# Performance work log

Hardware: AMD Instinct MI355X
Metric: run time of the kernel (lower is better)

Reference implementation:

```python
import jax, jax.numpy as jnp
import numpy as np

HIDDEN = 2048
NUM_HEADS = 16
NUM_KV_HEADS = 4
HEAD_DIM = HIDDEN // NUM_HEADS  # 128
GROUP = NUM_HEADS // NUM_KV_HEADS  # 4
SCALE = HEAD_DIM ** -0.5


def setup_inputs() -> dict:
    key = jax.random.key(0)
    ks = jax.random.split(key, 9)
    B, S = 2, 2048
    kv_dim = HEAD_DIM * NUM_KV_HEADS
    std = HIDDEN ** -0.5
    return {
        "x": jax.random.normal(ks[0], (B, S, HIDDEN), dtype=jnp.float32),
        "Wq": jax.random.normal(ks[1], (HIDDEN, HIDDEN), dtype=jnp.float32) * std,
        "bq": jnp.zeros((HIDDEN,), dtype=jnp.float32),
        "Wk": jax.random.normal(ks[2], (HIDDEN, kv_dim), dtype=jnp.float32) * std,
        "bk": jnp.zeros((kv_dim,), dtype=jnp.float32),
        "Wv": jax.random.normal(ks[3], (HIDDEN, kv_dim), dtype=jnp.float32) * std,
        "bv": jnp.zeros((kv_dim,), dtype=jnp.float32),
        "Wo": jax.random.normal(ks[4], (HIDDEN, HIDDEN), dtype=jnp.float32) * std,
        "bo": jnp.zeros((HIDDEN,), dtype=jnp.float32),
    }


def reference(x, Wq, bq, Wk, bk, Wv, bv, Wo, bo):
    B, S, _ = x.shape
    # projections
    q = (x @ Wq + bq).reshape(B, S, NUM_KV_HEADS, GROUP, HEAD_DIM)  # grouped query heads
    k = (x @ Wk + bk).reshape(B, S, NUM_KV_HEADS, HEAD_DIM)
    v = (x @ Wv + bv).reshape(B, S, NUM_KV_HEADS, HEAD_DIM)
    # scores: [B, Hkv, G, Sq, Sk] -- same math as repeat_interleave of K/V over G,
    # but K/V are broadcast over the group axis instead of materialized.
    attn = jnp.einsum("bqhgd,bkhd->bhgqk", q, k) * SCALE
    attn = jax.nn.softmax(attn, axis=-1)
    out = jnp.einsum("bhgqk,bkhd->bqhgd", attn, v).reshape(B, S, HIDDEN)
    return out @ Wo + bo
```

## Files before the change

### kernel.cpp

```cpp
#include <hip/hip_runtime.h>


#define SEQ    2048
#define HIDDEN 2048

typedef __attribute__((ext_vector_type(8))) short v8s;
typedef __attribute__((ext_vector_type(4))) float v4f;

#define MFMA16(a,b,c) __builtin_amdgcn_mfma_f32_16x16x32_bf16((a),(b),(c),0,0,0)

__device__ __forceinline__ ushort f2b(float f){
  unsigned u = __float_as_uint(f);
  u += 0x7fffu + ((u >> 16) & 1u);
  return (ushort)(u >> 16);
}

__device__ __forceinline__ void gload16(const void* g, void* l){
  __builtin_amdgcn_global_load_lds((const __attribute__((address_space(1))) void*)g,
                                   (__attribute__((address_space(3))) void*)l, 16, 0, 0);
}

#define WAIT_VM0   0x0F70
#define WAIT_LGKM0 0xC07F

__global__ void k_conv(const float* __restrict__ in, ushort* __restrict__ out, int n){
  int i = (blockIdx.x*256 + threadIdx.x)*4;
  if (i >= n) return;
  float4 f = *(const float4*)(in + i);
  ushort4 u; u.x=f2b(f.x); u.y=f2b(f.y); u.z=f2b(f.z); u.w=f2b(f.w);
  *(ushort4*)(out + i) = u;
}

__global__ void k_tconv(const float* __restrict__ in, ushort* __restrict__ out,
                        int rows, int cols){
  __shared__ float t[32][33];
  int tx = threadIdx.x & 31, ty = threadIdx.x >> 5;
  int c0 = blockIdx.x*32, r0 = blockIdx.y*32;
#pragma unroll
  for (int i=0;i<4;i++) t[ty+i*8][tx] = in[(size_t)(r0+ty+i*8)*cols + c0+tx];
  __syncthreads();
#pragma unroll
  for (int i=0;i<4;i++) out[(size_t)(c0+ty+i*8)*rows + r0+tx] = f2b(t[tx][ty+i*8]);
}

__global__ void k_tv(const ushort* __restrict__ vb, ushort* __restrict__ vT){
  __shared__ ushort t[32][33];
  int tx = threadIdx.x & 31, ty = threadIdx.x >> 5;
  int s0 = blockIdx.x*32, d0 = blockIdx.y*32, bh = blockIdx.z;
  int b = bh >> 2, h = bh & 3;
  const ushort* src = vb + (size_t)b*SEQ*512 + h*128;
#pragma unroll
  for (int i=0;i<4;i++) t[ty+i*8][tx] = src[(size_t)(s0+ty+i*8)*512 + d0+tx];
  __syncthreads();
  ushort* dst = vT + (size_t)bh*128*SEQ;
#pragma unroll
  for (int i=0;i<4;i++) dst[(size_t)(d0+ty+i*8)*SEQ + s0+tx] = t[tx][ty+i*8];
}

#define GEMM_MAIN(A_, Bt_, K_)                                                        \
  __shared__ ushort sA[128*32], sB[128*32];                                           \
  const int tid = threadIdx.x, lane = tid & 63, wid = tid >> 6;                       \
  const int wm = wid >> 1, wn = wid & 1, lm = lane & 15, q8 = (lane >> 4)*8;          \
  const int rowB = blockIdx.y*128, colB = blockIdx.x*128;                             \
  v4f acc[4][4] = {};                                                                 \
  for (int k0 = 0; k0 < (K_); k0 += 32){                                              \
    _Pragma("unroll")                                                                 \
    for (int it=0; it<2; it++){                                                       \
      int c = tid + it*256;                                                           \
      gload16((A_)  + (size_t)(rowB + (c>>2))*(K_) + k0 + (c&3)*8, (char*)sA + c*16); \
      gload16((Bt_) + (size_t)(colB + (c>>2))*(K_) + k0 + (c&3)*8, (char*)sB + c*16); \
    }                                                                                 \
    __syncthreads();                                                                  \
    v8s af[4], bfr[4];                                                                \
    _Pragma("unroll")                                                                 \
    for (int i=0;i<4;i++){                                                            \
      af[i]  = *(const v8s*)(sA + (wm*64 + i*16 + lm)*32 + q8);                       \
      bfr[i] = *(const v8s*)(sB + (wn*64 + i*16 + lm)*32 + q8);                       \
    }                                                                                 \
    _Pragma("unroll")                                                                 \
    for (int i=0;i<4;i++)                                                             \
      _Pragma("unroll")                                                               \
      for (int j=0;j<4;j++) acc[i][j] = MFMA16(af[i], bfr[j], acc[i][j]);             \
    __syncthreads();                                                                  \
  }                                                                                   \
  const int quad = lane >> 4;

__global__ __launch_bounds__(256) void k_gemm_qkv(
    const ushort* __restrict__ A, const ushort* __restrict__ Bt,
    const float* __restrict__ bq, const float* __restrict__ bk, const float* __restrict__ bv,
    ushort* __restrict__ qb, ushort* __restrict__ kb, ushort* __restrict__ vb){
  GEMM_MAIN(A, Bt, HIDDEN)
#pragma unroll
  for (int i=0;i<4;i++)
#pragma unroll
  for (int j=0;j<4;j++){
    int col = colB + wn*64 + j*16 + lm;
#pragma unroll
    for (int r=0;r<4;r++){
      int row = rowB + wm*64 + i*16 + quad*4 + r;
      float v = acc[i][j][r];
      if (col < 2048)      qb[(size_t)row*2048 + col]        = f2b(v + bq[col]);
      else if (col < 2560) kb[(size_t)row*512 + (col-2048)]  = f2b(v + bk[col-2048]);
      else                 vb[(size_t)row*512 + (col-2560)]  = f2b(v + bv[col-2560]);
    }
  }
}

__global__ __launch_bounds__(256) void k_gemm_out(
    const ushort* __restrict__ A, const ushort* __restrict__ Bt,
    const float* __restrict__ bo, float* __restrict__ out){
  GEMM_MAIN(A, Bt, HIDDEN)
#pragma unroll
  for (int i=0;i<4;i++)
#pragma unroll
  for (int j=0;j<4;j++){
    int col = colB + wn*64 + j*16 + lm;
#pragma unroll
    for (int r=0;r<4;r++){
      int row = rowB + wm*64 + i*16 + quad*4 + r;
      out[(size_t)row*2048 + col] = acc[i][j][r] + bo[col];
    }
  }
}

__global__ __launch_bounds__(512, 1) void k_attn(
    const ushort* __restrict__ qb, const ushort* __restrict__ kb,
    const ushort* __restrict__ vT, ushort* __restrict__ Ob){
  __shared__ ushort sK[2][64*128];
  __shared__ ushort sV[2][128*64];
  __shared__ ushort sP[8][2048];
  const int tid = threadIdx.x, lane = tid & 63, w = tid >> 6;
  const int lm = lane & 15, quad = lane >> 4, q8 = quad*8;
  const int pair = blockIdx.x & 7;
  const int hkv = pair & 3, b = pair >> 2;
  const int qt = (blockIdx.x >> 3) & 7, g = blockIdx.x >> 6;
  const int head = hkv*4 + g;
  const float C = 0.08838834764831845f * 1.4426950408889634f;

  const ushort* kbb = kb + (size_t)b*SEQ*512 + hkv*128;
  const ushort* vbb = vT + (size_t)(b*4+hkv)*128*SEQ;

  const int kk = lane >> 4, ksw = lane & 15;
  const int dd = lane >> 3, vsw = lane & 7;

#define STAGE_K(t, buf) { _Pragma("unroll") for (int i=0;i<2;i++){                     \
    int c = w*2 + i; int key = c*4 + kk; int wd = ksw ^ (key & 15);                    \
    gload16(kbb + (size_t)((t)*64 + key)*512 + wd*8, &sK[buf][c*512 + lane*8]); } }
#define STAGE_V(t, buf) { _Pragma("unroll") for (int i=0;i<2;i++){                     \
    int c = w*2 + i; int drow = c*8 + dd; int wd = vsw ^ dd;                           \
    gload16(vbb + (size_t)drow*SEQ + (t)*64 + wd*8, &sV[buf][c*512 + lane*8]); } }

  v8s qf[2][4];
#pragma unroll
  for (int rb=0; rb<2; rb++)
#pragma unroll
    for (int ks=0; ks<4; ks++)
      qf[rb][ks] = *(const v8s*)(qb + (size_t)(b*SEQ + qt*256 + w*32 + rb*16 + lm)*HIDDEN
                                    + head*128 + ks*32 + q8);

  v4f o[2][8] = {};
  float lreg[2] = {0.f, 0.f};

  STAGE_K(0, 0)
  STAGE_V(0, 0)
  __builtin_amdgcn_s_waitcnt(WAIT_VM0);
  __syncthreads();

  for (int t=0; t<32; t++){
    const int cur = t & 1;
    if (t < 31) STAGE_K(t+1, cur^1)

    v8s kf[4][4];
#pragma unroll
    for (int kt=0; kt<4; kt++)
#pragma unroll
      for (int ks=0; ks<4; ks++)
        kf[kt][ks] = *(const v8s*)(&sK[cur][(kt*16+lm)*128 + ((ks*4+quad)^lm)*8]);

    v4f sacc[2][4] = {};
    __builtin_amdgcn_s_setprio(1);
#pragma unroll
    for (int ks=0; ks<4; ks++)
#pragma unroll
      for (int kt=0; kt<4; kt++)
#pragma unroll
        for (int rb=0; rb<2; rb++)
          sacc[rb][kt] = MFMA16(kf[kt][ks], qf[rb][ks], sacc[rb][kt]);
    __builtin_amdgcn_s_setprio(0);

#pragma unroll
    for (int rb=0; rb<2; rb++){
      float rs = 0.f;
#pragma unroll
      for (int kt=0; kt<4; kt++){
        float p0 = __builtin_amdgcn_exp2f(sacc[rb][kt][0]*C);
        float p1 = __builtin_amdgcn_exp2f(sacc[rb][kt][1]*C);
        float p2 = __builtin_amdgcn_exp2f(sacc[rb][kt][2]*C);
        float p3 = __builtin_amdgcn_exp2f(sacc[rb][kt][3]*C);
        rs += (p0+p1)+(p2+p3);
        uint2 pk;
        pk.x = (unsigned)f2b(p0) | ((unsigned)f2b(p1) << 16);
        pk.y = (unsigned)f2b(p2) | ((unsigned)f2b(p3) << 16);
        int kc = kt >> 1;
        int dl = ((kt&1)*2 + (quad>>1))*16 + lm;
        *(uint2*)(&sP[w][(rb*2+kc)*512 + dl*8 + (quad&1)*4]) = pk;
      }
      lreg[rb] += rs;
    }

    __builtin_amdgcn_s_waitcnt(WAIT_VM0);
    __syncthreads();
    if (t < 31) STAGE_V(t+1, cur^1)

    __builtin_amdgcn_s_waitcnt(WAIT_LGKM0);
    v8s pa[2][2];
#pragma unroll
    for (int rb=0; rb<2; rb++)
#pragma unroll
      for (int kc=0; kc<2; kc++)
        pa[rb][kc] = *(const v8s*)(&sP[w][(rb*2+kc)*512 + lane*8]);
    v8s vf[8][2];
#pragma unroll
    for (int dt=0; dt<8; dt++)
#pragma unroll
      for (int kc=0; kc<2; kc++)
        vf[dt][kc] = *(const v8s*)(&sV[cur][(dt*16+lm)*64 + ((kc*4+quad)^(lm&7))*8]);
    __builtin_amdgcn_s_setprio(1);
#pragma unroll
    for (int kc=0; kc<2; kc++)
#pragma unroll
      for (int dt=0; dt<8; dt++)
#pragma unroll
        for (int rb=0; rb<2; rb++)
          o[rb][dt] = MFMA16(pa[rb][kc], vf[dt][kc], o[rb][dt]);
    __builtin_amdgcn_s_setprio(0);
  }

#pragma unroll
  for (int rb=0; rb<2; rb++){
    float lv = lreg[rb];
    lv += __shfl_xor(lv, 16);
    lv += __shfl_xor(lv, 32);
    float inv[4];
#pragma unroll
    for (int r=0;r<4;r++) inv[r] = 1.0f / __shfl(lv, (lane & 48) + quad*4 + r);
#pragma unroll
    for (int dt=0; dt<8; dt++)
#pragma unroll
      for (int r=0;r<4;r++){
        int row = b*SEQ + qt*256 + w*32 + rb*16 + quad*4 + r;
        int col = head*128 + dt*16 + lm;
        Ob[(size_t)row*HIDDEN + col] = f2b(o[rb][dt][r]*inv[r]);
      }
  }
#undef STAGE_K
#undef STAGE_V
}

extern "C" void kernel_launch(void* const* d_in, const int* in_sizes, int n_in,
                              void* d_out, int out_size, void* d_ws, size_t ws_size,
                              hipStream_t stream){
  const float* x  = (const float*)d_in[0];
  const float* Wq = (const float*)d_in[1];
  const float* bq = (const float*)d_in[2];
  const float* Wk = (const float*)d_in[3];
  const float* bk = (const float*)d_in[4];
  const float* Wv = (const float*)d_in[5];
  const float* bv = (const float*)d_in[6];
  const float* Wo = (const float*)d_in[7];
  const float* bo = (const float*)d_in[8];
  float* out = (float*)d_out;

  ushort* xb  = (ushort*)d_ws;
  ushort* Wt  = xb  + 8388608;
  ushort* Wto = Wt  + 6291456;
  ushort* qb  = Wto + 4194304;
  ushort* kb  = qb  + 8388608;
  ushort* vb  = kb  + 2097152;
  ushort* vT  = vb  + 2097152;
  ushort* Ob  = vT  + 2097152;

  k_conv <<<8192, 256, 0, stream>>>(x, xb, 8388608);
  k_tconv<<<dim3(64,64), 256, 0, stream>>>(Wq, Wt, 2048, 2048);
  k_tconv<<<dim3(16,64), 256, 0, stream>>>(Wk, Wt + 4194304, 2048, 512);
  k_tconv<<<dim3(16,64), 256, 0, stream>>>(Wv, Wt + 5242880, 2048, 512);
  k_tconv<<<dim3(64,64), 256, 0, stream>>>(Wo, Wto, 2048, 2048);
  k_gemm_qkv<<<dim3(24,32), 256, 0, stream>>>(xb, Wt, bq, bk, bv, qb, kb, vb);
  k_tv  <<<dim3(64,4,8), 256, 0, stream>>>(vb, vT);
  k_attn<<<256, 512, 0, stream>>>(qb, kb, vT, Ob);
  k_gemm_out<<<dim3(16,32), 256, 0, stream>>>(Ob, Wto, bo, out);
}
```

Before: 327.3 us.

## Halve attention query tile per block, double grid, use packed bf16 convert

The attention kernel now gives each wave 16 query rows instead of 32, so a block covers 128 queries and the grid doubles to 512 blocks. The P scratch buffer shrinks to match, and launch bounds are raised so more blocks can share a CU. Probability packing switches to the hardware v_cvt_pk_bf16_f32 instruction instead of manual rounding. This improves occupancy and latency hiding, but each K/V tile loaded into shared memory is now reused by half as many queries, doubling K/V traffic.

```diff
diff --git a/kernel.cpp b/kernel.cpp
--- a/kernel.cpp
+++ b/kernel.cpp
@@ -13,6 +13,12 @@
   unsigned u = __float_as_uint(f);
   u += 0x7fffu + ((u >> 16) & 1u);
   return (ushort)(u >> 16);
+}
+
+__device__ __forceinline__ unsigned cvt_pk_bf16(float lo, float hi){
+  unsigned r;
+  asm("v_cvt_pk_bf16_f32 %0, %1, %2" : "=v"(r) : "v"(lo), "v"(hi));
+  return r;
 }
 
 __device__ __forceinline__ void gload16(const void* g, void* l){
@@ -123,17 +129,17 @@
   }
 }
 
-__global__ __launch_bounds__(512, 1) void k_attn(
+__global__ __launch_bounds__(512, 4) void k_attn(
     const ushort* __restrict__ qb, const ushort* __restrict__ kb,
     const ushort* __restrict__ vT, ushort* __restrict__ Ob){
   __shared__ ushort sK[2][64*128];
   __shared__ ushort sV[2][128*64];
-  __shared__ ushort sP[8][2048];
+  __shared__ ushort sP[8][1024];
   const int tid = threadIdx.x, lane = tid & 63, w = tid >> 6;
   const int lm = lane & 15, quad = lane >> 4, q8 = quad*8;
   const int pair = blockIdx.x & 7;
   const int hkv = pair & 3, b = pair >> 2;
-  const int qt = (blockIdx.x >> 3) & 7, g = blockIdx.x >> 6;
+  const int qt = (blockIdx.x >> 3) & 15, g = blockIdx.x >> 7;
   const int head = hkv*4 + g;
   const float C = 0.08838834764831845f * 1.4426950408889634f;
 
@@ -150,16 +156,14 @@
     int c = w*2 + i; int drow = c*8 + dd; int wd = vsw ^ dd;                           \
     gload16(vbb + (size_t)drow*SEQ + (t)*64 + wd*8, &sV[buf][c*512 + lane*8]); } }
 
-  v8s qf[2][4];
-#pragma unroll
-  for (int rb=0; rb<2; rb++)
-#pragma unroll
-    for (int ks=0; ks<4; ks++)
-      qf[rb][ks] = *(const v8s*)(qb + (size_t)(b*SEQ + qt*256 + w*32 + rb*16 + lm)*HIDDEN
-                                    + head*128 + ks*32 + q8);
-
-  v4f o[2][8] = {};
-  float lreg[2] = {0.f, 0.f};
+  v8s qf[4];
+#pragma unroll
+  for (int ks=0; ks<4; ks++)
+    qf[ks] = *(const v8s*)(qb + (size_t)(b*SEQ + qt*128 + w*16 + lm)*HIDDEN
+                              + head*128 + ks*32 + q8);
+
+  v4f o[8] = {};
+  float lreg = 0.f;
 
   STAGE_K(0, 0)
   STAGE_V(0, 0)
@@ -177,35 +181,32 @@
       for (int ks=0; ks<4; ks++)
         kf[kt][ks] = *(const v8s*)(&sK[cur][(kt*16+lm)*128 + ((ks*4+quad)^lm)*8]);
 
-    v4f sacc[2][4] = {};
+    v4f sacc[4] = {};
     __builtin_amdgcn_s_setprio(1);
 #pragma unroll
     for (int ks=0; ks<4; ks++)
 #pragma unroll
       for (int kt=0; kt<4; kt++)
-#pragma unroll
-        for (int rb=0; rb<2; rb++)
-          sacc[rb][kt] = MFMA16(kf[kt][ks], qf[rb][ks], sacc[rb][kt]);
+        sacc[kt] = MFMA16(kf[kt][ks], qf[ks], sacc[kt]);
     __builtin_amdgcn_s_setprio(0);
 
-#pragma unroll
-    for (int rb=0; rb<2; rb++){
+    {
       float rs = 0.f;
 #pragma unroll
       for (int kt=0; kt<4; kt++){
-        float p0 = __builtin_amdgcn_exp2f(sacc[rb][kt][0]*C);
-        float p1 = __builtin_amdgcn_exp2f(sacc[rb][kt][1]*C);
-        float p2 = __builtin_amdgcn_exp2f(sacc[rb][kt][2]*C);
-        float p3 = __builtin_amdgcn_exp2f(sacc[rb][kt][3]*C);
+        float p0 = __builtin_amdgcn_exp2f(sacc[kt][0]*C);
+        float p1 = __builtin_amdgcn_exp2f(sacc[kt][1]*C);
+        float p2 = __builtin_amdgcn_exp2f(sacc[kt][2]*C);
+        float p3 = __builtin_amdgcn_exp2f(sacc[kt][3]*C);
         rs += (p0+p1)+(p2+p3);
         uint2 pk;
-        pk.x = (unsigned)f2b(p0) | ((unsigned)f2b(p1) << 16);
-        pk.y = (unsigned)f2b(p2) | ((unsigned)f2b(p3) << 16);
+        pk.x = cvt_pk_bf16(p0, p1);
+        pk.y = cvt_pk_bf16(p2, p3);
         int kc = kt >> 1;
         int dl = ((kt&1)*2 + (quad>>1))*16 + lm;
-        *(uint2*)(&sP[w][(rb*2+kc)*512 + dl*8 + (quad&1)*4]) = pk;
+        *(uint2*)(&sP[w][kc*512 + dl*8 + (quad&1)*4]) = pk;
       }
-      lreg[rb] += rs;
+      lreg += rs;
     }
 
     __builtin_amdgcn_s_waitcnt(WAIT_VM0);
@@ -213,12 +214,10 @@
     if (t < 31) STAGE_V(t+1, cur^1)
 
     __builtin_amdgcn_s_waitcnt(WAIT_LGKM0);
-    v8s pa[2][2];
-#pragma unroll
-    for (int rb=0; rb<2; rb++)
-#pragma unroll
-      for (int kc=0; kc<2; kc++)
-        pa[rb][kc] = *(const v8s*)(&sP[w][(rb*2+kc)*512 + lane*8]);
+    v8s pa[2];
+#pragma unroll
+    for (int kc=0; kc<2; kc++)
+      pa[kc] = *(const v8s*)(&sP[w][kc*512 + lane*8]);
     v8s vf[8][2];
 #pragma unroll
     for (int dt=0; dt<8; dt++)
@@ -230,15 +229,12 @@
     for (int kc=0; kc<2; kc++)
 #pragma unroll
       for (int dt=0; dt<8; dt++)
-#pragma unroll
-        for (int rb=0; rb<2; rb++)
-          o[rb][dt] = MFMA16(pa[rb][kc], vf[dt][kc], o[rb][dt]);
+        o[dt] = MFMA16(pa[kc], vf[dt][kc], o[dt]);
     __builtin_amdgcn_s_setprio(0);
   }
 
-#pragma unroll
-  for (int rb=0; rb<2; rb++){
-    float lv = lreg[rb];
+  {
+    float lv = lreg;
     lv += __shfl_xor(lv, 16);
     lv += __shfl_xor(lv, 32);
     float inv[4];
@@ -248,9 +244,9 @@
     for (int dt=0; dt<8; dt++)
 #pragma unroll
       for (int r=0;r<4;r++){
-        int row = b*SEQ + qt*256 + w*32 + rb*16 + quad*4 + r;
+        int row = b*SEQ + qt*128 + w*16 + quad*4 + r;
         int col = head*128 + dt*16 + lm;
-        Ob[(size_t)row*HIDDEN + col] = f2b(o[rb][dt][r]*inv[r]);
+        Ob[(size_t)row*HIDDEN + col] = f2b(o[dt][r]*inv[r]);
       }
   }
 #undef STAGE_K
@@ -287,6 +283,6 @@
   k_tconv<<<dim3(64,64), 256, 0, stream>>>(Wo, Wto, 2048, 2048);
   k_gemm_qkv<<<dim3(24,32), 256, 0, stream>>>(xb, Wt, bq, bk, bv, qb, kb, vb);
   k_tv  <<<dim3(64,4,8), 256, 0, stream>>>(vb, vT);
-  k_attn<<<256, 512, 0, stream>>>(qb, kb, vT, Ob);
+  k_attn<<<512, 512, 0, stream>>>(qb, kb, vT, Ob);
   k_gemm_out<<<dim3(16,32), 256, 0, stream>>>(Ob, Wto, bo, out);
 }
```

Result: slower. 347.3 us (+6.1%).
